# Optimization experiments

Measured on AMD Instinct MI355X. Metric: run time of the kernel, lower is better.

## Reference

```python
import jax, jax.numpy as jnp
import numpy as np

# ---- hash-grid encoder constants (instant-ngp / tiny-cuda-nn style) ----
L = 24          # nr_levels (hard-coded in Density.__init__)
F = 2           # features per level -> output_dim = 48
T = 2 ** 19     # hashmap size per level
BASE_RES = 16
FINEST_RES = 2048
_b = np.exp(np.log(FINEST_RES / BASE_RES) / (L - 1))
RES = np.floor(BASE_RES * _b ** np.arange(L)).astype(np.float32)  # [L]
PRIMES = np.array([1, 2654435761, 805459861], dtype=np.uint32)
OFFS = np.array([[(i >> d) & 1 for d in range(3)] for i in range(8)], dtype=np.int32)  # [8,3] cube corners


def hash_encode(points, hash_table, bb_sides):
    """points [N,3] in [-bb/2, bb/2]; hash_table [L,T,F] -> [N, L*F]."""
    x = jnp.clip(points / bb_sides + 0.5, 0.0, 1.0)  # normalize to unit cube

    def level_fn(_, lv):
        tbl, res = lv                     # tbl [T,F], res scalar
        pos = x * res                     # [N,3]
        i0 = jnp.floor(pos)
        w = pos - i0                      # [N,3] trilinear weights
        corner = i0.astype(jnp.uint32)[:, None, :] + jnp.asarray(OFFS, jnp.uint32)[None]  # [N,8,3]
        hp = corner * jnp.asarray(PRIMES)[None, None, :]
        h = (hp[..., 0] ^ hp[..., 1] ^ hp[..., 2]) & jnp.uint32(T - 1)  # [N,8]
        wts = jnp.where(jnp.asarray(OFFS, bool)[None], w[:, None, :], 1.0 - w[:, None, :]).prod(-1)  # [N,8]
        feat = tbl[h]                     # gather [N,8,F]
        return 0, (wts[..., None] * feat).sum(axis=1)  # [N,F]

    _, feats = jax.lax.scan(level_fn, 0, (hash_table, jnp.asarray(RES)))  # [L,N,F]
    return jnp.transpose(feats, (1, 0, 2)).reshape(points.shape[0], L * F)


def setup_inputs() -> dict:
    key = jax.random.key(0)
    ks = jax.random.split(key, 8)
    N = 1048576
    points = jax.random.uniform(ks[0], (N, 3), dtype=jnp.float32) * 2.0 - 1.0  # in bb [-1,1]^3
    bb_sides = jnp.full((3,), 2.0, dtype=jnp.float32)
    hash_table = jax.random.uniform(ks[1], (L, T, F), dtype=jnp.float32, minval=-1e-4, maxval=1e-4)
    d_enc, d_h, d_out = L * F, 64, 33  # 1 density + 32 geom feats
    w1 = jax.random.normal(ks[2], (d_enc, d_h), dtype=jnp.float32) / np.sqrt(d_enc)
    b1 = jnp.zeros((d_h,), jnp.float32)
    w2 = jax.random.normal(ks[3], (d_h, d_h), dtype=jnp.float32) / np.sqrt(d_h)
    b2 = jnp.zeros((d_h,), jnp.float32)
    w3 = jax.random.normal(ks[4], (d_h, d_out), dtype=jnp.float32) / np.sqrt(d_h)
    b3 = jnp.zeros((d_out,), jnp.float32)
    return {"points": points, "bb_sides": bb_sides, "hash_table": hash_table,
            "w1": w1, "b1": b1, "w2": w2, "b2": b2, "w3": w3, "b3": b3}


def reference(points, bb_sides, hash_table, w1, b1, w2, b2, w3, b3):
    enc = hash_encode(points, hash_table, bb_sides)        # [N,48]
    h = jax.nn.relu(enc @ w1 + b1)
    h = jax.nn.relu(h @ w2 + b2)
    out = h @ w3 + b3                                      # [N,33], last layer linear
    density = jax.nn.softplus(out[:, 0:1])                 # [N,1]
    geom_feat = out[:, 1:]                                 # [N,32]
    return density, geom_feat
```

## Files before the change

### kernel.cpp

```cpp
#include <hip/hip_runtime.h>
#include <math.h>

#define TSZ 524288u
#define TMASK 524287u

#define WPACK 5808
#define ENC_OFF 8192

struct ResTab { float v[24]; };

typedef __attribute__((ext_vector_type(8))) short frag_ab;
typedef __attribute__((ext_vector_type(4))) float frag_cd;

union FU { uint4 u; frag_ab f; };

static __device__ __forceinline__ frag_ab ldfrag(const unsigned int* p) {
    FU x; x.u = *(const uint4*)p; return x.f;
}
static __device__ __forceinline__ float bf2f(unsigned int u) {
    return __uint_as_float(u << 16);
}
static __device__ __forceinline__ unsigned short f2bf(float f) {
    unsigned int u = __float_as_uint(f);
    unsigned int r = (u + 0x7fffu + ((u >> 16) & 1u)) >> 16;
    return (unsigned short)r;
}
static __device__ __forceinline__ float lo16(unsigned int d) { return __uint_as_float(d << 16); }
static __device__ __forceinline__ float hi16(unsigned int d) { return __uint_as_float(d & 0xffff0000u); }

template<bool F32>
static __device__ __forceinline__ float ld(const void* p, int i) {
    if constexpr (F32) return ((const float*)p)[i];
    else return bf2f((unsigned int)((const unsigned short*)p)[i]);
}

static __device__ __forceinline__ frag_cd mfma(frag_ab a, frag_ab b, frag_cd c) {
    return __builtin_amdgcn_mfma_f32_16x16x32_bf16(a, b, c, 0, 0, 0);
}

template<bool F32>
static __device__ __forceinline__ unsigned int encode_one(
    float x0, float x1, float x2, float rr, const void* tbl, int l)
{
    float p0 = x0 * rr, p1 = x1 * rr, p2 = x2 * rr;
    float f0 = floorf(p0), f1 = floorf(p1), f2 = floorf(p2);
    float w0 = p0 - f0, w1v = p1 - f1, w2v = p2 - f2;
    unsigned int i0 = (unsigned int)f0, i1 = (unsigned int)f1, i2 = (unsigned int)f2;
    unsigned int ax0 = i0, ax1 = i0 + 1u;
    unsigned int ay0 = i1 * 2654435761u, ay1 = ay0 + 2654435761u;
    unsigned int az0 = i2 * 805459861u,  az1 = az0 + 805459861u;
    unsigned int h0 = (ax0 ^ ay0 ^ az0) & TMASK;
    unsigned int h1 = (ax1 ^ ay0 ^ az0) & TMASK;
    unsigned int h2 = (ax0 ^ ay1 ^ az0) & TMASK;
    unsigned int h3 = (ax1 ^ ay1 ^ az0) & TMASK;
    unsigned int h4 = (ax0 ^ ay0 ^ az1) & TMASK;
    unsigned int h5 = (ax1 ^ ay0 ^ az1) & TMASK;
    unsigned int h6 = (ax0 ^ ay1 ^ az1) & TMASK;
    unsigned int h7 = (ax1 ^ ay1 ^ az1) & TMASK;

    float g0l, g0h, g1l, g1h, g2l, g2h, g3l, g3h;
    float g4l, g4h, g5l, g5h, g6l, g6h, g7l, g7h;
    if constexpr (F32) {
        const float2* lt = (const float2*)tbl + (size_t)l * TSZ;
        float2 d0 = lt[h0], d1 = lt[h1], d2 = lt[h2], d3 = lt[h3];
        float2 d4 = lt[h4], d5 = lt[h5], d6 = lt[h6], d7 = lt[h7];
        g0l = d0.x; g0h = d0.y; g1l = d1.x; g1h = d1.y;
        g2l = d2.x; g2h = d2.y; g3l = d3.x; g3h = d3.y;
        g4l = d4.x; g4h = d4.y; g5l = d5.x; g5h = d5.y;
        g6l = d6.x; g6h = d6.y; g7l = d7.x; g7h = d7.y;
    } else {
        const unsigned int* lt = (const unsigned int*)tbl + (size_t)l * TSZ;
        unsigned int d0 = lt[h0], d1 = lt[h1], d2 = lt[h2], d3 = lt[h3];
        unsigned int d4 = lt[h4], d5 = lt[h5], d6 = lt[h6], d7 = lt[h7];
        g0l = lo16(d0); g0h = hi16(d0); g1l = lo16(d1); g1h = hi16(d1);
        g2l = lo16(d2); g2h = hi16(d2); g3l = lo16(d3); g3h = hi16(d3);
        g4l = lo16(d4); g4h = hi16(d4); g5l = lo16(d5); g5h = hi16(d5);
        g6l = lo16(d6); g6h = hi16(d6); g7l = lo16(d7); g7h = hi16(d7);
    }

    float v0 = 1.f - w0, v1 = 1.f - w1v, v2 = 1.f - w2v;
    float wy0z0 = v1 * v2,  wy1z0 = w1v * v2;
    float wy0z1 = v1 * w2v, wy1z1 = w1v * w2v;
    float c0 = v0 * wy0z0, c1 = w0 * wy0z0, c2 = v0 * wy1z0, c3 = w0 * wy1z0;
    float c4 = v0 * wy0z1, c5 = w0 * wy0z1, c6 = v0 * wy1z1, c7 = w0 * wy1z1;
    float e0 = c0 * g0l + c1 * g1l + c2 * g2l + c3 * g3l
             + c4 * g4l + c5 * g5l + c6 * g6l + c7 * g7l;
    float e1 = c0 * g0h + c1 * g1h + c2 * g2h + c3 * g3h
             + c4 * g4h + c5 * g5h + c6 * g6h + c7 * g7h;
    return (unsigned int)f2bf(e0) | (((unsigned int)f2bf(e1)) << 16);
}

static __device__ __forceinline__ void hidden_layer(
    const unsigned int* Wu, const float* Bv, frag_ab A[4][2],
    unsigned int* sAu, int wv, int li, int qq)
{
#pragma unroll
    for (int nt = 0; nt < 4; ++nt) {
        frag_ab Bf0 = ldfrag(&Wu[(((nt * 16 + li) * 8) + (qq ^ (li & 7))) * 4]);
        frag_ab Bf1 = ldfrag(&Wu[(((nt * 16 + li) * 8) + ((4 + qq) ^ (li & 7))) * 4]);
        float bias = Bv[nt * 16 + li];
#pragma unroll
        for (int m = 0; m < 4; ++m) {
            frag_cd c = {0.f, 0.f, 0.f, 0.f};
            c = mfma(A[m][0], Bf0, c);
            c = mfma(A[m][1], Bf1, c);
            int dst4 = ((wv * 4 + m) * 2 + (nt >> 1)) * 64 + ((nt * 2 + (li >> 3)) & 3) * 16;
#pragma unroll
            for (int r = 0; r < 4; ++r) {
                float v = fmaxf(c[r] + bias, 0.f);
                unsigned int mybf = f2bf(v);
                unsigned int oth = (unsigned int)(unsigned short)__shfl_xor((int)mybf, 1, 64);
                if (!(li & 1))
                    sAu[(dst4 + qq * 4 + r) * 4 + ((li & 7) >> 1)] = mybf | (oth << 16);
            }
        }
    }
}

static __device__ __forceinline__ void mlp_tail(
    const unsigned int* Wf1, const unsigned int* Wf2, const unsigned int* Wf3,
    const float* Bf1, const float* Bf2, const float* Bf3,
    float* out, int N, unsigned int* sAu)
{
    const int t  = threadIdx.x;
    const int ln = t & 63;
    const int wv = t >> 6;
    const int li = t & 15;
    const int qq = ln >> 4;

    frag_ab A[4][2];
#pragma unroll
    for (int m = 0; m < 4; ++m)
#pragma unroll
        for (int ks = 0; ks < 2; ++ks)
            A[m][ks] = ldfrag(&sAu[((((wv * 4 + m) * 2) + ks) * 64 + ln) * 4]);

    hidden_layer(Wf1, Bf1, A, sAu, wv, li, qq);
    __syncthreads();
#pragma unroll
    for (int m = 0; m < 4; ++m)
#pragma unroll
        for (int ks = 0; ks < 2; ++ks)
            A[m][ks] = ldfrag(&sAu[((((wv * 4 + m) * 2) + ks) * 64 + ln) * 4]);

    hidden_layer(Wf2, Bf2, A, sAu, wv, li, qq);
    __syncthreads();
#pragma unroll
    for (int m = 0; m < 4; ++m)
#pragma unroll
        for (int ks = 0; ks < 2; ++ks)
            A[m][ks] = ldfrag(&sAu[((((wv * 4 + m) * 2) + ks) * 64 + ln) * 4]);

#pragma unroll
    for (int nt = 0; nt < 3; ++nt) {
        frag_ab Bf0 = ldfrag(&Wf3[(((nt * 16 + li) * 8) + (qq ^ (li & 7))) * 4]);
        frag_ab Bf1 = ldfrag(&Wf3[(((nt * 16 + li) * 8) + ((4 + qq) ^ (li & 7))) * 4]);
        float bias = Bf3[nt * 16 + li];
        int col = nt * 16 + li;
#pragma unroll
        for (int m = 0; m < 4; ++m) {
            frag_cd c = {0.f, 0.f, 0.f, 0.f};
            c = mfma(A[m][0], Bf0, c);
            c = mfma(A[m][1], Bf1, c);
#pragma unroll
            for (int r = 0; r < 4; ++r) {
                float v = c[r] + bias;
                unsigned int mybf = f2bf(v);
                unsigned int oth = (unsigned int)(unsigned short)__shfl_xor((int)mybf, 1, 64);
                if (!(li & 1) && col < 33)
                    sAu[wv * 2048 + (m * 16 + qq * 4 + r) * 17 + (col >> 1)] = mybf | (oth << 16);
            }
        }
    }

    __syncthreads();

    {
        int p2 = blockIdx.x * 256 + t;
        const unsigned int* rowp = &sAu[(t >> 6) * 2048 + (t & 63) * 17];
        unsigned int u[17];
#pragma unroll
        for (int j = 0; j < 17; ++j) u[j] = rowp[j];
        if (p2 < N) {
            float v0 = bf2f(u[0] & 0xffffu);
            float sp = (v0 > 20.f) ? v0 : log1pf(expf(v0));
            out[p2] = sp;
            float g[32];
#pragma unroll
            for (int k = 0; k < 32; ++k) {
                int c = k + 1;
                unsigned int h = (c & 1) ? (u[c >> 1] >> 16) : (u[c >> 1] & 0xffffu);
                g[k] = bf2f(h);
            }
            float* og = out + N + (size_t)p2 * 32;
#pragma unroll
            for (int k = 0; k < 32; k += 4) {
                float4 q; q.x = g[k]; q.y = g[k + 1]; q.z = g[k + 2]; q.w = g[k + 3];
                *(float4*)&og[k] = q;
            }
        }
    }
}

static __device__ __forceinline__ void zero_pad_rows(unsigned int* sAu) {
    const int t  = threadIdx.x;
    const int wv = t >> 6;
    const int mt = (t >> 4) & 3;
    const int li = t & 15;
    uint4 z; z.x = 0u; z.y = 0u; z.z = 0u; z.w = 0u;
    int u2 = ((wv * 4 + mt) * 2 + 1) * 64 + 2 * 16 + li;
    int u3 = ((wv * 4 + mt) * 2 + 1) * 64 + 3 * 16 + li;
    *(uint4*)&sAu[u2 * 4] = z;
    *(uint4*)&sAu[u3 * 4] = z;
}


template<bool F32>
static __device__ __forceinline__ void gather_body(
    const void* points, const void* bb, const void* tbl,
    unsigned int* enc, int N, int nB, const ResTab& rt)
{
    const int t = threadIdx.x;
    int l  = blockIdx.x / nB;
    int bx = blockIdx.x - l * nB;
    int p  = bx * 256 + t;
    int pc = (p < N) ? p : (N - 1);
    float ptx = ld<F32>(points, pc * 3 + 0);
    float pty = ld<F32>(points, pc * 3 + 1);
    float ptz = ld<F32>(points, pc * 3 + 2);
    float x0 = fminf(fmaxf(ptx / ld<F32>(bb, 0) + 0.5f, 0.f), 1.f);
    float x1 = fminf(fmaxf(pty / ld<F32>(bb, 1) + 0.5f, 0.f), 1.f);
    float x2 = fminf(fmaxf(ptz / ld<F32>(bb, 2) + 0.5f, 0.f), 1.f);

    unsigned int pk = encode_one<F32>(x0, x1, x2, rt.v[l], tbl, l);
    __builtin_nontemporal_store(pk, &enc[((size_t)l * nB + bx) * 256 + t]);
}

__global__ __launch_bounds__(256) void ngp_gather(
    const void* __restrict__ points, const void* __restrict__ bb,
    const void* __restrict__ tbl, unsigned int* __restrict__ enc,
    int N, int nB, ResTab rt)
{
    bool isF32 = (((const unsigned int*)bb)[0] == 0x40000000u);
    if (isF32) gather_body<true>(points, bb, tbl, enc, N, nB, rt);
    else       gather_body<false>(points, bb, tbl, enc, N, nB, rt);
}

__global__ __launch_bounds__(256, 4) void ngp_mlp(
    const unsigned int* __restrict__ enc, const unsigned int* __restrict__ wp,
    float* __restrict__ out, int N, int nB)
{
    __shared__ unsigned int sAu[8192];

    const int t  = threadIdx.x;
    const int ln = t & 63;
    const int wv = t >> 6;
    const int mt = (t >> 4) & 3;
    const int li = t & 15;

    zero_pad_rows(sAu);

    const int rowBase = ((wv * 4 + mt) * 2) * 64 + li;
#pragma unroll
    for (int l = 0; l < 24; ++l) {
        unsigned int pk = __builtin_nontemporal_load(
            &enc[((size_t)l * nB + blockIdx.x) * 256 + t]);
        sAu[(rowBase + (l >> 4) * 64 + ((l >> 2) & 3) * 16) * 4 + (l & 3)] = pk;
    }

    __syncthreads();

    mlp_tail(wp, wp + 2048, wp + 4096,
             (const float*)(wp + 5632), (const float*)(wp + 5696),
             (const float*)(wp + 5760), out, N, sAu);
}

template<bool F32>
static __device__ __forceinline__ void pack_body(
    const void* w1, const void* b1, const void* w2, const void* b2,
    const void* w3, const void* b3, unsigned int* wp)
{
    const int t = threadIdx.x;
    unsigned int* W1 = wp;
    unsigned int* W2 = wp + 2048;
    unsigned int* W3 = wp + 4096;
    float* B1 = (float*)(wp + 5632);
    float* B2 = (float*)(wp + 5696);
    float* B3 = (float*)(wp + 5760);

    for (int idx = t; idx < 2048; idx += 256) {
        int n = idx & 63, k0 = (idx >> 6) * 2;
        unsigned int lo1 = (k0     < 48) ? f2bf(ld<F32>(w1, k0 * 64 + n))       : 0u;
        unsigned int hi1 = (k0 + 1 < 48) ? f2bf(ld<F32>(w1, (k0 + 1) * 64 + n)) : 0u;
        unsigned int lo2 = f2bf(ld<F32>(w2, k0 * 64 + n));
        unsigned int hi2 = f2bf(ld<F32>(w2, (k0 + 1) * 64 + n));
        int dst = (n * 8 + ((k0 >> 3) ^ (n & 7))) * 4 + ((k0 & 7) >> 1);
        W1[dst] = lo1 | (hi1 << 16);
        W2[dst] = lo2 | (hi2 << 16);
    }
    for (int idx = t; idx < 1536; idx += 256) {
        int n = idx >> 5, k0 = (idx & 31) * 2;
        unsigned int lo = (n < 33) ? f2bf(ld<F32>(w3, k0 * 33 + n))       : 0u;
        unsigned int hi = (n < 33) ? f2bf(ld<F32>(w3, (k0 + 1) * 33 + n)) : 0u;
        int dst = (n * 8 + ((k0 >> 3) ^ (n & 7))) * 4 + ((k0 & 7) >> 1);
        W3[dst] = lo | (hi << 16);
    }
    if (t < 64) { B1[t] = ld<F32>(b1, t); B2[t] = ld<F32>(b2, t); }
    if (t < 48) B3[t] = (t < 33) ? ld<F32>(b3, t) : 0.f;
}

__global__ void pack_weights(
    const void* __restrict__ bb,
    const void* __restrict__ w1, const void* __restrict__ b1,
    const void* __restrict__ w2, const void* __restrict__ b2,
    const void* __restrict__ w3, const void* __restrict__ b3,
    unsigned int* __restrict__ wp)
{
    bool isF32 = (((const unsigned int*)bb)[0] == 0x40000000u);
    if (isF32) pack_body<true>(w1, b1, w2, b2, w3, b3, wp);
    else       pack_body<false>(w1, b1, w2, b2, w3, b3, wp);
}


template<bool F32>
static __device__ __forceinline__ void body_lds(
    const void* points, const void* bb, const void* tbl,
    const void* w1, const void* b1, const void* w2, const void* b2,
    const void* w3, const void* b3,
    float* out, int N, const ResTab& rt,
    unsigned int* sAu, unsigned int* sW1u, unsigned int* sW2u, unsigned int* sW3u,
    float* sB1, float* sB2, float* sB3)
{
    const int t  = threadIdx.x;
    const int wv = t >> 6;
    const int mt = (t >> 4) & 3;
    const int li = t & 15;

    for (int idx = t; idx < 2048; idx += 256) {
        int n = idx & 63, k0 = (idx >> 6) * 2;
        unsigned int lo1 = (k0     < 48) ? f2bf(ld<F32>(w1, k0 * 64 + n))       : 0u;
        unsigned int hi1 = (k0 + 1 < 48) ? f2bf(ld<F32>(w1, (k0 + 1) * 64 + n)) : 0u;
        unsigned int lo2 = f2bf(ld<F32>(w2, k0 * 64 + n));
        unsigned int hi2 = f2bf(ld<F32>(w2, (k0 + 1) * 64 + n));
        int dst = (n * 8 + ((k0 >> 3) ^ (n & 7))) * 4 + ((k0 & 7) >> 1);
        sW1u[dst] = lo1 | (hi1 << 16);
        sW2u[dst] = lo2 | (hi2 << 16);
    }
    for (int idx = t; idx < 1536; idx += 256) {
        int n = idx >> 5, k0 = (idx & 31) * 2;
        unsigned int lo = (n < 33) ? f2bf(ld<F32>(w3, k0 * 33 + n))       : 0u;
        unsigned int hi = (n < 33) ? f2bf(ld<F32>(w3, (k0 + 1) * 33 + n)) : 0u;
        int dst = (n * 8 + ((k0 >> 3) ^ (n & 7))) * 4 + ((k0 & 7) >> 1);
        sW3u[dst] = lo | (hi << 16);
    }
    if (t < 64) { sB1[t] = ld<F32>(b1, t); sB2[t] = ld<F32>(b2, t); }
    if (t < 48) sB3[t] = (t < 33) ? ld<F32>(b3, t) : 0.f;

    zero_pad_rows(sAu);

    int p  = blockIdx.x * 256 + t;
    int pc = (p < N) ? p : (N - 1);
    float ptx = ld<F32>(points, pc * 3 + 0);
    float pty = ld<F32>(points, pc * 3 + 1);
    float ptz = ld<F32>(points, pc * 3 + 2);
    float x0 = fminf(fmaxf(ptx / ld<F32>(bb, 0) + 0.5f, 0.f), 1.f);
    float x1 = fminf(fmaxf(pty / ld<F32>(bb, 1) + 0.5f, 0.f), 1.f);
    float x2 = fminf(fmaxf(ptz / ld<F32>(bb, 2) + 0.5f, 0.f), 1.f);

    const int rowBase = ((wv * 4 + mt) * 2) * 64 + li;

#pragma unroll 4
    for (int l = 0; l < 24; ++l) {
        unsigned int pk = encode_one<F32>(x0, x1, x2, rt.v[l], tbl, l);
        sAu[(rowBase + (l >> 4) * 64 + ((l >> 2) & 3) * 16) * 4 + (l & 3)] = pk;
    }

    __syncthreads();

    mlp_tail(sW1u, sW2u, sW3u, sB1, sB2, sB3, out, N, sAu);
}

__global__ __launch_bounds__(256, 2) void ngp_fused(
    const void* __restrict__ points, const void* __restrict__ bb,
    const void* __restrict__ tbl,
    const void* __restrict__ w1, const void* __restrict__ b1,
    const void* __restrict__ w2, const void* __restrict__ b2,
    const void* __restrict__ w3, const void* __restrict__ b3,
    float* __restrict__ out, int N, ResTab rt)
{
    __shared__ unsigned int sAu[8192];
    __shared__ unsigned int sW1u[2048];
    __shared__ unsigned int sW2u[2048];
    __shared__ unsigned int sW3u[1536];
    __shared__ float sB1[64], sB2[64], sB3[48];

    bool isF32 = (((const unsigned int*)bb)[0] == 0x40000000u);
    if (isF32)
        body_lds<true>(points, bb, tbl, w1, b1, w2, b2, w3, b3, out, N, rt,
                       sAu, sW1u, sW2u, sW3u, sB1, sB2, sB3);
    else
        body_lds<false>(points, bb, tbl, w1, b1, w2, b2, w3, b3, out, N, rt,
                        sAu, sW1u, sW2u, sW3u, sB1, sB2, sB3);
}

extern "C" void kernel_launch(void* const* d_in, const int* in_sizes, int n_in,
                              void* d_out, int out_size, void* d_ws, size_t ws_size,
                              hipStream_t stream) {
    const void* points = nullptr; const void* bb = nullptr; const void* tbl = nullptr;
    const void* w1 = nullptr; const void* b1 = nullptr;
    const void* w2 = nullptr; const void* b2 = nullptr;
    const void* w3 = nullptr; const void* b3 = nullptr;

    int iTbl = -1, iPts = -1;
    long sTbl = -1, sPts = -1;
    for (int i = 0; i < n_in; ++i) {
        long s = in_sizes[i];
        if (s > sTbl) { sPts = sTbl; iPts = iTbl; sTbl = s; iTbl = i; }
        else if (s > sPts) { sPts = s; iPts = i; }
    }
    tbl = d_in[iTbl];
    points = d_in[iPts];
    for (int i = 0; i < n_in; ++i) {
        if (i == iTbl || i == iPts) continue;
        int s = in_sizes[i];
        if      (s == 4096) w2 = d_in[i];
        else if (s == 3072) w1 = d_in[i];
        else if (s == 2112) w3 = d_in[i];
        else if (s == 33)   b3 = d_in[i];
        else if (s == 3)    bb = d_in[i];
        else if (s == 64)   { if (!b1) b1 = d_in[i]; else b2 = d_in[i]; }
    }

    int N = (int)(sPts / 3);

    ResTab rt;
    double bexp = exp(log(2048.0 / 16.0) / 23.0);
    for (int l = 0; l < 24; ++l)
        rt.v[l] = (float)floor(16.0 * pow(bexp, (double)l));

    int nb = (N + 255) / 256;
    size_t need = ((size_t)ENC_OFF + (size_t)24 * nb * 256) * 4;

    if (d_ws && ws_size >= need) {
        unsigned int* wp  = (unsigned int*)d_ws;
        unsigned int* enc = wp + ENC_OFF;
        pack_weights<<<1, 256, 0, stream>>>(bb, w1, b1, w2, b2, w3, b3, wp);
        ngp_gather<<<nb * 24, 256, 0, stream>>>(points, bb, tbl, enc, N, nb, rt);
        ngp_mlp<<<nb, 256, 0, stream>>>(enc, wp, (float*)d_out, N, nb);
    } else {
        ngp_fused<<<nb, 256, 0, stream>>>(points, bb, tbl, w1, b1, w2, b2, w3, b3,
                                          (float*)d_out, N, rt);
    }
}
```

Measured before the change: 886.0 us.

## Pair adjacent-x hash corners into wide loads and coalesce MLP output stores

```diff
diff --git a/kernel.cpp b/kernel.cpp
--- a/kernel.cpp
+++ b/kernel.cpp
@@ -62,20 +62,44 @@
     float g4l, g4h, g5l, g5h, g6l, g6h, g7l, g7h;
     if constexpr (F32) {
         const float2* lt = (const float2*)tbl + (size_t)l * TSZ;
-        float2 d0 = lt[h0], d1 = lt[h1], d2 = lt[h2], d3 = lt[h3];
-        float2 d4 = lt[h4], d5 = lt[h5], d6 = lt[h6], d7 = lt[h7];
-        g0l = d0.x; g0h = d0.y; g1l = d1.x; g1h = d1.y;
-        g2l = d2.x; g2h = d2.y; g3l = d3.x; g3h = d3.y;
-        g4l = d4.x; g4h = d4.y; g5l = d5.x; g5h = d5.y;
-        g6l = d6.x; g6h = d6.y; g7l = d7.x; g7h = d7.y;
+        float4 dA = *(const float4*)&lt[h0 & ~1u];
+        float4 dB = *(const float4*)&lt[h2 & ~1u];
+        float4 dC = *(const float4*)&lt[h4 & ~1u];
+        float4 dD = *(const float4*)&lt[h6 & ~1u];
+        g0l = (h0 & 1u) ? dA.z : dA.x;  g0h = (h0 & 1u) ? dA.w : dA.y;
+        g2l = (h2 & 1u) ? dB.z : dB.x;  g2h = (h2 & 1u) ? dB.w : dB.y;
+        g4l = (h4 & 1u) ? dC.z : dC.x;  g4h = (h4 & 1u) ? dC.w : dC.y;
+        g6l = (h6 & 1u) ? dD.z : dD.x;  g6h = (h6 & 1u) ? dD.w : dD.y;
+        g1l = (h0 & 1u) ? dA.x : dA.z;  g1h = (h0 & 1u) ? dA.y : dA.w;
+        g3l = (h2 & 1u) ? dB.x : dB.z;  g3h = (h2 & 1u) ? dB.y : dB.w;
+        g5l = (h4 & 1u) ? dC.x : dC.z;  g5h = (h4 & 1u) ? dC.y : dC.w;
+        g7l = (h6 & 1u) ? dD.x : dD.z;  g7h = (h6 & 1u) ? dD.y : dD.w;
+        if (i0 & 1u) {
+            float2 e1 = lt[h1], e3 = lt[h3], e5 = lt[h5], e7 = lt[h7];
+            g1l = e1.x; g1h = e1.y; g3l = e3.x; g3h = e3.y;
+            g5l = e5.x; g5h = e5.y; g7l = e7.x; g7h = e7.y;
+        }
     } else {
         const unsigned int* lt = (const unsigned int*)tbl + (size_t)l * TSZ;
-        unsigned int d0 = lt[h0], d1 = lt[h1], d2 = lt[h2], d3 = lt[h3];
-        unsigned int d4 = lt[h4], d5 = lt[h5], d6 = lt[h6], d7 = lt[h7];
-        g0l = lo16(d0); g0h = hi16(d0); g1l = lo16(d1); g1h = hi16(d1);
-        g2l = lo16(d2); g2h = hi16(d2); g3l = lo16(d3); g3h = hi16(d3);
-        g4l = lo16(d4); g4h = hi16(d4); g5l = lo16(d5); g5h = hi16(d5);
-        g6l = lo16(d6); g6h = hi16(d6); g7l = lo16(d7); g7h = hi16(d7);
+        uint2 dA = *(const uint2*)&lt[h0 & ~1u];
+        uint2 dB = *(const uint2*)&lt[h2 & ~1u];
+        uint2 dC = *(const uint2*)&lt[h4 & ~1u];
+        uint2 dD = *(const uint2*)&lt[h6 & ~1u];
+        unsigned int u0 = (h0 & 1u) ? dA.y : dA.x;
+        unsigned int u1 = (h0 & 1u) ? dA.x : dA.y;
+        unsigned int u2 = (h2 & 1u) ? dB.y : dB.x;
+        unsigned int u3 = (h2 & 1u) ? dB.x : dB.y;
+        unsigned int u4 = (h4 & 1u) ? dC.y : dC.x;
+        unsigned int u5 = (h4 & 1u) ? dC.x : dC.y;
+        unsigned int u6 = (h6 & 1u) ? dD.y : dD.x;
+        unsigned int u7 = (h6 & 1u) ? dD.x : dD.y;
+        if (i0 & 1u) {
+            u1 = lt[h1]; u3 = lt[h3]; u5 = lt[h5]; u7 = lt[h7];
+        }
+        g0l = lo16(u0); g0h = hi16(u0); g1l = lo16(u1); g1h = hi16(u1);
+        g2l = lo16(u2); g2h = hi16(u2); g3l = lo16(u3); g3h = hi16(u3);
+        g4l = lo16(u4); g4h = hi16(u4); g5l = lo16(u5); g5h = hi16(u5);
+        g6l = lo16(u6); g6h = hi16(u6); g7l = lo16(u7); g7h = hi16(u7);
     }
 
     float v0 = 1.f - w0, v1 = 1.f - w1v, v2 = 1.f - w2v;
@@ -176,28 +200,29 @@
     __syncthreads();
 
     {
-        int p2 = blockIdx.x * 256 + t;
-        const unsigned int* rowp = &sAu[(t >> 6) * 2048 + (t & 63) * 17];
-        unsigned int u[17];
-#pragma unroll
-        for (int j = 0; j < 17; ++j) u[j] = rowp[j];
-        if (p2 < N) {
-            float v0 = bf2f(u[0] & 0xffffu);
+        int bStart = blockIdx.x * 256;
+        {
+            unsigned int u0 = sAu[(t >> 6) * 2048 + (t & 63) * 17];
+            float v0 = bf2f(u0 & 0xffffu);
             float sp = (v0 > 20.f) ? v0 : log1pf(expf(v0));
-            out[p2] = sp;
-            float g[32];
-#pragma unroll
-            for (int k = 0; k < 32; ++k) {
-                int c = k + 1;
-                unsigned int h = (c & 1) ? (u[c >> 1] >> 16) : (u[c >> 1] & 0xffffu);
-                g[k] = bf2f(h);
-            }
-            float* og = out + N + (size_t)p2 * 32;
-#pragma unroll
-            for (int k = 0; k < 32; k += 4) {
-                float4 q; q.x = g[k]; q.y = g[k + 1]; q.z = g[k + 2]; q.w = g[k + 3];
-                *(float4*)&og[k] = q;
-            }
+            if (bStart + t < N) out[bStart + t] = sp;
+        }
+        float* og = out + N + (size_t)bStart * 32;
+#pragma unroll
+        for (int i = 0; i < 8; ++i) {
+            int j  = i * 1024 + t * 4;
+            int pt = j >> 5;
+            int c  = j & 31;
+            const unsigned int* rp = &sAu[(pt >> 6) * 2048 + (pt & 63) * 17];
+            unsigned int a0 = rp[(c >> 1)];
+            unsigned int a1 = rp[(c >> 1) + 1];
+            unsigned int a2 = rp[(c >> 1) + 2];
+            float4 q;
+            q.x = bf2f(a0 >> 16);
+            q.y = bf2f(a1 & 0xffffu);
+            q.z = bf2f(a1 >> 16);
+            q.w = bf2f(a2 & 0xffffu);
+            if (bStart + pt < N) *(float4*)&og[j] = q;
         }
     }
 }
@@ -253,7 +278,6 @@
     __shared__ unsigned int sAu[8192];
 
     const int t  = threadIdx.x;
-    const int ln = t & 63;
     const int wv = t >> 6;
     const int mt = (t >> 4) & 3;
     const int li = t & 15;
@@ -263,8 +287,7 @@
     const int rowBase = ((wv * 4 + mt) * 2) * 64 + li;
 #pragma unroll
     for (int l = 0; l < 24; ++l) {
-        unsigned int pk = __builtin_nontemporal_load(
-            &enc[((size_t)l * nB + blockIdx.x) * 256 + t]);
+        unsigned int pk = enc[((size_t)l * nB + blockIdx.x) * 256 + t];
         sAu[(rowBase + (l >> 4) * 64 + ((l >> 2) & 3) * 16) * 4 + (l & 3)] = pk;
     }
 
```

After: 924.2 us. +4.3%, slower.

## Process two points per gather thread and coalesce MLP output stores

Applied to the files above, without the earlier changes.

```diff
diff --git a/kernel.cpp b/kernel.cpp
--- a/kernel.cpp
+++ b/kernel.cpp
@@ -176,28 +176,29 @@
     __syncthreads();
 
     {
-        int p2 = blockIdx.x * 256 + t;
-        const unsigned int* rowp = &sAu[(t >> 6) * 2048 + (t & 63) * 17];
-        unsigned int u[17];
-#pragma unroll
-        for (int j = 0; j < 17; ++j) u[j] = rowp[j];
-        if (p2 < N) {
-            float v0 = bf2f(u[0] & 0xffffu);
+        int bStart = blockIdx.x * 256;
+        {
+            unsigned int u0 = sAu[(t >> 6) * 2048 + (t & 63) * 17];
+            float v0 = bf2f(u0 & 0xffffu);
             float sp = (v0 > 20.f) ? v0 : log1pf(expf(v0));
-            out[p2] = sp;
-            float g[32];
-#pragma unroll
-            for (int k = 0; k < 32; ++k) {
-                int c = k + 1;
-                unsigned int h = (c & 1) ? (u[c >> 1] >> 16) : (u[c >> 1] & 0xffffu);
-                g[k] = bf2f(h);
-            }
-            float* og = out + N + (size_t)p2 * 32;
-#pragma unroll
-            for (int k = 0; k < 32; k += 4) {
-                float4 q; q.x = g[k]; q.y = g[k + 1]; q.z = g[k + 2]; q.w = g[k + 3];
-                *(float4*)&og[k] = q;
-            }
+            if (bStart + t < N) out[bStart + t] = sp;
+        }
+        float* og = out + N + (size_t)bStart * 32;
+#pragma unroll
+        for (int i = 0; i < 8; ++i) {
+            int j  = i * 1024 + t * 4;
+            int pt = j >> 5;
+            int c  = j & 31;
+            const unsigned int* rp = &sAu[(pt >> 6) * 2048 + (pt & 63) * 17];
+            unsigned int a0 = rp[(c >> 1)];
+            unsigned int a1 = rp[(c >> 1) + 1];
+            unsigned int a2 = rp[(c >> 1) + 2];
+            float4 q;
+            q.x = bf2f(a0 >> 16);
+            q.y = bf2f(a1 & 0xffffu);
+            q.z = bf2f(a1 >> 16);
+            q.w = bf2f(a2 & 0xffffu);
+            if (bStart + pt < N) *(float4*)&og[j] = q;
         }
     }
 }
@@ -218,42 +219,56 @@
 template<bool F32>
 static __device__ __forceinline__ void gather_body(
     const void* points, const void* bb, const void* tbl,
-    unsigned int* enc, int N, int nB, const ResTab& rt)
+    unsigned int* enc, int N, size_t Np, int nB2, const ResTab& rt)
 {
     const int t = threadIdx.x;
-    int l  = blockIdx.x / nB;
-    int bx = blockIdx.x - l * nB;
-    int p  = bx * 256 + t;
-    int pc = (p < N) ? p : (N - 1);
-    float ptx = ld<F32>(points, pc * 3 + 0);
-    float pty = ld<F32>(points, pc * 3 + 1);
-    float ptz = ld<F32>(points, pc * 3 + 2);
-    float x0 = fminf(fmaxf(ptx / ld<F32>(bb, 0) + 0.5f, 0.f), 1.f);
-    float x1 = fminf(fmaxf(pty / ld<F32>(bb, 1) + 0.5f, 0.f), 1.f);
-    float x2 = fminf(fmaxf(ptz / ld<F32>(bb, 2) + 0.5f, 0.f), 1.f);
-
-    unsigned int pk = encode_one<F32>(x0, x1, x2, rt.v[l], tbl, l);
-    __builtin_nontemporal_store(pk, &enc[((size_t)l * nB + bx) * 256 + t]);
+    int l  = blockIdx.x / nB2;
+    int bx = blockIdx.x - l * nB2;
+    int p0 = bx * 512 + t;
+    int p1 = p0 + 256;
+    int pc0 = (p0 < N) ? p0 : (N - 1);
+    int pc1 = (p1 < N) ? p1 : (N - 1);
+
+    float ax = ld<F32>(points, pc0 * 3 + 0);
+    float ay = ld<F32>(points, pc0 * 3 + 1);
+    float az = ld<F32>(points, pc0 * 3 + 2);
+    float bx_ = ld<F32>(points, pc1 * 3 + 0);
+    float by_ = ld<F32>(points, pc1 * 3 + 1);
+    float bz_ = ld<F32>(points, pc1 * 3 + 2);
+    float ib0 = 1.f / ld<F32>(bb, 0);
+    float ib1 = 1.f / ld<F32>(bb, 1);
+    float ib2 = 1.f / ld<F32>(bb, 2);
+    float xa0 = fminf(fmaxf(ax * ib0 + 0.5f, 0.f), 1.f);
+    float xa1 = fminf(fmaxf(ay * ib1 + 0.5f, 0.f), 1.f);
+    float xa2 = fminf(fmaxf(az * ib2 + 0.5f, 0.f), 1.f);
+    float xb0 = fminf(fmaxf(bx_ * ib0 + 0.5f, 0.f), 1.f);
+    float xb1 = fminf(fmaxf(by_ * ib1 + 0.5f, 0.f), 1.f);
+    float xb2 = fminf(fmaxf(bz_ * ib2 + 0.5f, 0.f), 1.f);
+
+    const float rr = rt.v[l];
+    unsigned int pk0 = encode_one<F32>(xa0, xa1, xa2, rr, tbl, l);
+    unsigned int pk1 = encode_one<F32>(xb0, xb1, xb2, rr, tbl, l);
+    __builtin_nontemporal_store(pk0, &enc[(size_t)l * Np + p0]);
+    __builtin_nontemporal_store(pk1, &enc[(size_t)l * Np + p1]);
 }
 
 __global__ __launch_bounds__(256) void ngp_gather(
     const void* __restrict__ points, const void* __restrict__ bb,
     const void* __restrict__ tbl, unsigned int* __restrict__ enc,
-    int N, int nB, ResTab rt)
+    int N, unsigned long long Np, int nB2, ResTab rt)
 {
     bool isF32 = (((const unsigned int*)bb)[0] == 0x40000000u);
-    if (isF32) gather_body<true>(points, bb, tbl, enc, N, nB, rt);
-    else       gather_body<false>(points, bb, tbl, enc, N, nB, rt);
+    if (isF32) gather_body<true>(points, bb, tbl, enc, N, (size_t)Np, nB2, rt);
+    else       gather_body<false>(points, bb, tbl, enc, N, (size_t)Np, nB2, rt);
 }
 
 __global__ __launch_bounds__(256, 4) void ngp_mlp(
     const unsigned int* __restrict__ enc, const unsigned int* __restrict__ wp,
-    float* __restrict__ out, int N, int nB)
+    float* __restrict__ out, int N, unsigned long long Np)
 {
     __shared__ unsigned int sAu[8192];
 
     const int t  = threadIdx.x;
-    const int ln = t & 63;
     const int wv = t >> 6;
     const int mt = (t >> 4) & 3;
     const int li = t & 15;
@@ -263,8 +278,7 @@
     const int rowBase = ((wv * 4 + mt) * 2) * 64 + li;
 #pragma unroll
     for (int l = 0; l < 24; ++l) {
-        unsigned int pk = __builtin_nontemporal_load(
-            &enc[((size_t)l * nB + blockIdx.x) * 256 + t]);
+        unsigned int pk = enc[(size_t)l * Np + blockIdx.x * 256 + t];
         sAu[(rowBase + (l >> 4) * 64 + ((l >> 2) & 3) * 16) * 4 + (l & 3)] = pk;
     }
 
@@ -438,15 +452,18 @@
     for (int l = 0; l < 24; ++l)
         rt.v[l] = (float)floor(16.0 * pow(bexp, (double)l));
 
-    int nb = (N + 255) / 256;
-    size_t need = ((size_t)ENC_OFF + (size_t)24 * nb * 256) * 4;
+    int nb  = (N + 255) / 256;
+    int nB2 = (N + 511) / 512;
+    unsigned long long Np = (unsigned long long)nB2 * 512;
+    size_t need = ((size_t)ENC_OFF + (size_t)24 * Np) * 4;
 
     if (d_ws && ws_size >= need) {
         unsigned int* wp  = (unsigned int*)d_ws;
         unsigned int* enc = wp + ENC_OFF;
         pack_weights<<<1, 256, 0, stream>>>(bb, w1, b1, w2, b2, w3, b3, wp);
-        ngp_gather<<<nb * 24, 256, 0, stream>>>(points, bb, tbl, enc, N, nb, rt);
-        ngp_mlp<<<nb, 256, 0, stream>>>(enc, wp, (float*)d_out, N, nb);
+        ngp_gather<<<nB2 * 24, 256, 0, stream>>>(points, bb, tbl, enc, N, Np, nB2, rt);
+        int nbm = (int)(Np / 256);
+        ngp_mlp<<<nbm, 256, 0, stream>>>(enc, wp, (float*)d_out, N, Np);
     } else {
         ngp_fused<<<nb, 256, 0, stream>>>(points, bb, tbl, w1, b1, w2, b2, w3, b3,
                                           (float*)d_out, N, rt);
```

Result: no change. 885.0 us (-0.1%).
